# Kernel tuning notes

Measured on AMD Instinct MI355X. Metric: run time of the kernel, lower is better.

## Reference

```python
import jax, jax.numpy as jnp
import numpy as np

N_NODES = 100000
N_EDGES = 1600000
NUM_FEATURES = 256
HIDDEN_DIM = 128
NUM_CLASSES = 16


def setup_inputs() -> dict:
    key = jax.random.key(0)
    k1, k2, k3, k4 = jax.random.split(key, 4)
    x = jax.random.normal(k1, (N_NODES, NUM_FEATURES), dtype=jnp.float32)
    edge_index = jax.random.randint(k2, (2, N_EDGES), 0, N_NODES, dtype=jnp.int64)
    # Glorot-style init like PyG GCNConv's Linear
    W1 = jax.random.normal(k3, (NUM_FEATURES, HIDDEN_DIM), dtype=jnp.float32) / np.sqrt(NUM_FEATURES)
    b1 = jnp.zeros((HIDDEN_DIM,), dtype=jnp.float32)
    W2 = jax.random.normal(k4, (HIDDEN_DIM, NUM_CLASSES), dtype=jnp.float32) / np.sqrt(HIDDEN_DIM)
    b2 = jnp.zeros((NUM_CLASSES,), dtype=jnp.float32)
    return {"x": x, "edge_index": edge_index, "W1": W1, "b1": b1, "W2": W2, "b2": b2}


def _gcn_norm(edge_index, num_nodes):
    """PyG GCNConv default: add self-loops, symmetric deg^{-1/2} A deg^{-1/2} norm."""
    loops = jnp.arange(num_nodes, dtype=edge_index.dtype)
    row = jnp.concatenate([edge_index[0], loops])  # source
    col = jnp.concatenate([edge_index[1], loops])  # target
    deg = jax.ops.segment_sum(jnp.ones_like(col, dtype=jnp.float32), col,
                              num_segments=num_nodes)
    dinv = jnp.where(deg > 0, jax.lax.rsqrt(deg), 0.0)
    norm = dinv[row] * dinv[col]  # [E + N]
    return row, col, norm


def _gcn_conv(h, row, col, norm, num_nodes):
    # transform first (PyG: lin then propagate), then normalized sum-aggregate
    msg = h[row] * norm[:, None]            # [E+N, d] gather + scale
    return jax.ops.segment_sum(msg, col, num_segments=num_nodes)


def reference(x, edge_index, W1, b1, W2, b2):
    num_nodes = x.shape[0]
    row, col, norm = _gcn_norm(edge_index, num_nodes)
    h = x @ W1
    h = _gcn_conv(h, row, col, norm, num_nodes) + b1
    h = jax.nn.relu(h)
    h = h @ W2
    out = _gcn_conv(h, row, col, norm, num_nodes) + b2
    return out
```

## Files before the change

### kernel.cpp

```cpp
#include <hip/hip_runtime.h>

#define N_NODES 100000
#define N_EDGES 1600000
#define F_IN    256
#define F_HID   128
#define F_OUT   16

#define BSHIFT  9
#define BNODES  512
#define NB      196
#define CHUNK   4096
#define NCHUNK  ((N_EDGES + CHUNK - 1) / CHUNK)

typedef __attribute__((ext_vector_type(8))) short short8;
typedef __attribute__((ext_vector_type(4))) float float4v;

__device__ __forceinline__ unsigned int bf16_rn(float f) {
    unsigned int u = __float_as_uint(f);
    return (u + 0x7FFFu + ((u >> 16) & 1u)) >> 16;
}
__device__ __forceinline__ unsigned int pk2(float lo, float hi) {
    return bf16_rn(lo) | (bf16_rn(hi) << 16);
}


__global__ __launch_bounds__(256) void k_bhist(const int* __restrict__ coli,
                                               int* __restrict__ bcnt) {
    __shared__ int lc[NB];
    int tid = threadIdx.x;
    for (int i = tid; i < NB; i += 256) lc[i] = 0;
    __syncthreads();
    for (int e = blockIdx.x * 256 + tid; e < N_EDGES; e += 256 * 256)
        atomicAdd(&lc[coli[e] >> BSHIFT], 1);
    __syncthreads();
    for (int i = tid; i < NB; i += 256)
        if (lc[i]) atomicAdd(&bcnt[i], lc[i]);
}

__global__ __launch_bounds__(256) void k_bscan(const int* __restrict__ bcnt,
                                               int* __restrict__ bbase,
                                               int* __restrict__ bcur) {
    __shared__ int sc[256];
    int t = threadIdx.x;
    int v = (t < NB) ? bcnt[t] : 0;
    sc[t] = v; __syncthreads();
    for (int off = 1; off < 256; off <<= 1) {
        int x = (t >= off) ? sc[t - off] : 0;
        __syncthreads();
        sc[t] += x;
        __syncthreads();
    }
    if (t < NB) {
        int e = sc[t] - v;
        bbase[t] = e;
        bcur[t]  = e;
    }
    if (t == 0) bbase[NB] = N_EDGES;
}

__global__ __launch_bounds__(256) void k_binscatter(const int* __restrict__ rowi,
                                                    const int* __restrict__ coli,
                                                    int* __restrict__ bcur,
                                                    int2* __restrict__ ebuf) {
    __shared__ int cnt[NB], gbase[NB], run[NB];
    int tid = threadIdx.x;
    int e0 = blockIdx.x * CHUNK;
    for (int i = tid; i < NB; i += 256) { cnt[i] = 0; run[i] = 0; }
    __syncthreads();
    int d[16], s[16];
    #pragma unroll
    for (int i = 0; i < 16; i++) {
        int e = e0 + i * 256 + tid;
        if (e < N_EDGES) {
            d[i] = coli[e]; s[i] = rowi[e];
            atomicAdd(&cnt[d[i] >> BSHIFT], 1);
        } else d[i] = -1;
    }
    __syncthreads();
    for (int i = tid; i < NB; i += 256)
        gbase[i] = cnt[i] ? atomicAdd(&bcur[i], cnt[i]) : 0;
    __syncthreads();
    #pragma unroll
    for (int i = 0; i < 16; i++) {
        if (d[i] >= 0) {
            int b = d[i] >> BSHIFT;
            int off = atomicAdd(&run[b], 1);
            ebuf[gbase[b] + off] = make_int2(d[i], s[i]);
        }
    }
}

__global__ __launch_bounds__(256) void k_finalize(const int* __restrict__ bbase,
                                                  const int2* __restrict__ ebuf,
                                                  int* __restrict__ row_ptr,
                                                  float* __restrict__ dinv,
                                                  int* __restrict__ esrc) {
    __shared__ int ndeg[BNODES];
    __shared__ int sc[BNODES];
    int tid = threadIdx.x;
    int b   = blockIdx.x;
    int nb0 = b << BSHIFT;
    int ebeg = bbase[b], eend = bbase[b + 1];
    ndeg[tid] = 0; ndeg[tid + 256] = 0;
    __syncthreads();
    for (int e = ebeg + tid; e < eend; e += 256)
        atomicAdd(&ndeg[ebuf[e].x - nb0], 1);
    __syncthreads();
    int i0 = tid, i1 = tid + 256;
    sc[i0] = ndeg[i0]; sc[i1] = ndeg[i1];
    __syncthreads();
    for (int off = 1; off < BNODES; off <<= 1) {
        int v0 = (i0 >= off) ? sc[i0 - off] : 0;
        int v1 = (i1 >= off) ? sc[i1 - off] : 0;
        __syncthreads();
        sc[i0] += v0; sc[i1] += v1;
        __syncthreads();
    }
    #pragma unroll
    for (int k = 0; k < 2; k++) {
        int i = tid + k * 256;
        int n = nb0 + i;
        int deg = ndeg[i];
        int excl = sc[i] - deg;
        if (n < N_NODES) {
            row_ptr[n] = ebeg + excl;
            dinv[n]    = rsqrtf(1.0f + (float)deg);
        }
        ndeg[i] = excl;
    }
    if (b == NB - 1 && tid == 0) row_ptr[N_NODES] = N_EDGES;
    __syncthreads();
    for (int e = ebeg + tid; e < eend; e += 256) {
        int2 p = ebuf[e];
        int off = atomicAdd(&ndeg[p.x - nb0], 1);
        esrc[ebeg + off] = p.y;
    }
}


__global__ __launch_bounds__(256) void k_transW(const float* __restrict__ W1,
                                                ushort* __restrict__ Wt) {
    int t = blockIdx.x * 256 + threadIdx.x;
    int c = t & 127, k = t >> 7;
    Wt[c * 256 + k] = (ushort)bf16_rn(W1[k * 128 + c]);
}


__global__ __launch_bounds__(256) void k_gemm1(const float* __restrict__ x,
                                               const ushort* __restrict__ Wt,
                                               const float* __restrict__ dinv,
                                               ushort* __restrict__ g1) {
    __shared__ ushort Al[128 * 40];
    __shared__ ushort Bl[128 * 40];
    const int tid = threadIdx.x;
    const int w = tid >> 6;
    const int l = tid & 63;
    const int m = l & 15;
    const int q = l >> 4;
    const int R0 = blockIdx.x * 128;

    const int srow = tid >> 1;
    const int soff = (tid & 1) * 16;

    int vr = R0 + srow; if (vr > N_NODES - 1) vr = N_NODES - 1;
    const float*  xrow = &x[(size_t)vr * F_IN + soff];
    const ushort* wrow = &Wt[srow * 256 + soff];

    float4v acc[2][8];
    #pragma unroll
    for (int i = 0; i < 2; i++)
        #pragma unroll
        for (int j = 0; j < 8; j++) acc[i][j] = (float4v){0.f, 0.f, 0.f, 0.f};

    for (int kt = 0; kt < F_IN; kt += 32) {
        float4 f0 = *(const float4*)&xrow[kt + 0];
        float4 f1 = *(const float4*)&xrow[kt + 4];
        float4 f2 = *(const float4*)&xrow[kt + 8];
        float4 f3 = *(const float4*)&xrow[kt + 12];
        uint4 wv0 = *(const uint4*)&wrow[kt + 0];
        uint4 wv1 = *(const uint4*)&wrow[kt + 8];
        uint4 pa, pb;
        pa.x = pk2(f0.x, f0.y); pa.y = pk2(f0.z, f0.w);
        pa.z = pk2(f1.x, f1.y); pa.w = pk2(f1.z, f1.w);
        pb.x = pk2(f2.x, f2.y); pb.y = pk2(f2.z, f2.w);
        pb.z = pk2(f3.x, f3.y); pb.w = pk2(f3.z, f3.w);
        *(uint4*)&Al[srow * 40 + soff]     = pa;
        *(uint4*)&Al[srow * 40 + soff + 8] = pb;
        *(uint4*)&Bl[srow * 40 + soff]     = wv0;
        *(uint4*)&Bl[srow * 40 + soff + 8] = wv1;
        __syncthreads();

        short8 af0 = *(const short8*)&Al[(w * 32 + m) * 40 + q * 8];
        short8 af1 = *(const short8*)&Al[(w * 32 + 16 + m) * 40 + q * 8];
        #pragma unroll
        for (int n = 0; n < 8; n++) {
            short8 bfr = *(const short8*)&Bl[(n * 16 + m) * 40 + q * 8];
            acc[0][n] = __builtin_amdgcn_mfma_f32_16x16x32_bf16(af0, bfr, acc[0][n], 0, 0, 0);
            acc[1][n] = __builtin_amdgcn_mfma_f32_16x16x32_bf16(af1, bfr, acc[1][n], 0, 0, 0);
        }
        __syncthreads();
    }

    const int rbase = R0 + w * 32 + q * 4;
    float dv0[4], dv1[4];
    #pragma unroll
    for (int r = 0; r < 4; r++) {
        int v0 = rbase + r;      dv0[r] = (v0 < N_NODES) ? dinv[v0] : 0.f;
        int v1 = rbase + 16 + r; dv1[r] = (v1 < N_NODES) ? dinv[v1] : 0.f;
    }
    #pragma unroll
    for (int n = 0; n < 8; n++) {
        #pragma unroll
        for (int r = 0; r < 4; r++) {
            int v0 = rbase + r;
            if (v0 < N_NODES)
                g1[v0 * F_HID + n * 16 + m] = (ushort)bf16_rn(dv0[r] * acc[0][n][r]);
            int v1 = rbase + 16 + r;
            if (v1 < N_NODES)
                g1[v1 * F_HID + n * 16 + m] = (ushort)bf16_rn(dv1[r] * acc[1][n][r]);
        }
    }
}


__global__ __launch_bounds__(256) void k_agg1(const int* __restrict__ row_ptr,
                                              const int* __restrict__ esrc,
                                              const float* __restrict__ dinv,
                                              const unsigned int* __restrict__ g1,
                                              const float* __restrict__ b1,
                                              float* __restrict__ h1b) {
    int node = blockIdx.x * 4 + (threadIdx.x >> 6);
    int lane = threadIdx.x & 63;
    if (node >= N_NODES) return;
    int s = row_ptr[node], t = row_ptr[node + 1];
    unsigned int u = g1[node * 64 + lane];
    float ax = __uint_as_float(u << 16);
    float ay = __uint_as_float(u & 0xFFFF0000u);
    int e = s;
    for (; e + 3 < t; e += 4) {
        int r0 = esrc[e], r1 = esrc[e + 1], r2 = esrc[e + 2], r3 = esrc[e + 3];
        unsigned int u0 = g1[r0 * 64 + lane];
        unsigned int u1 = g1[r1 * 64 + lane];
        unsigned int u2 = g1[r2 * 64 + lane];
        unsigned int u3 = g1[r3 * 64 + lane];
        ax += __uint_as_float(u0 << 16) + __uint_as_float(u1 << 16)
            + __uint_as_float(u2 << 16) + __uint_as_float(u3 << 16);
        ay += __uint_as_float(u0 & 0xFFFF0000u) + __uint_as_float(u1 & 0xFFFF0000u)
            + __uint_as_float(u2 & 0xFFFF0000u) + __uint_as_float(u3 & 0xFFFF0000u);
    }
    for (; e < t; e++) {
        unsigned int u0 = g1[esrc[e] * 64 + lane];
        ax += __uint_as_float(u0 << 16);
        ay += __uint_as_float(u0 & 0xFFFF0000u);
    }
    float wv = dinv[node];
    float2 bb = ((const float2*)b1)[lane];
    float2 o;
    o.x = fmaxf(fmaf(wv, ax, bb.x), 0.0f);
    o.y = fmaxf(fmaf(wv, ay, bb.y), 0.0f);
    ((float2*)h1b)[node * 64 + lane] = o;
}


__global__ __launch_bounds__(256) void k_gemm2(const float* __restrict__ h1b,
                                               const float* __restrict__ W2,
                                               const float* __restrict__ dinv,
                                               float* __restrict__ g2) {
    __shared__ float ls[64 * 129];
    __shared__ float ws2[F_HID * F_OUT];
    const int tid = threadIdx.x;
    const int v0  = blockIdx.x * 64;

    for (int i = tid; i < F_HID * F_OUT; i += 256) ws2[i] = W2[i];
    __syncthreads();

    #pragma unroll
    for (int i = 0; i < 32; i++) {
        int f = i * 256 + tid;
        int rr = f >> 7, cc = f & 127;
        int v = v0 + rr;
        ls[rr * 129 + cc] = (v < N_NODES) ? h1b[v * F_HID + cc] : 0.0f;
    }
    __syncthreads();

    const int v  = tid >> 2;
    const int cq = (tid & 3) * 4;
    float acc[4] = {0.f, 0.f, 0.f, 0.f};
    #pragma unroll 8
    for (int f = 0; f < F_HID; f++) {
        float a = ls[v * 129 + f];
        #pragma unroll
        for (int j = 0; j < 4; j++)
            acc[j] = fmaf(a, ws2[f * F_OUT + cq + j], acc[j]);
    }
    int vv = v0 + v;
    if (vv < N_NODES) {
        float w = dinv[vv];
        float4 t = make_float4(w * acc[0], w * acc[1], w * acc[2], w * acc[3]);
        *(float4*)&g2[vv * F_OUT + cq] = t;
    }
}


__global__ __launch_bounds__(256) void k_agg2(const int* __restrict__ row_ptr,
                                              const int* __restrict__ esrc,
                                              const float* __restrict__ dinv,
                                              const float* __restrict__ g2,
                                              const float* __restrict__ b2,
                                              float* __restrict__ out) {
    int gid = blockIdx.x * 256 + threadIdx.x;
    int node = gid >> 4;
    int f = gid & 15;
    if (node >= N_NODES) return;
    int s = row_ptr[node], t = row_ptr[node + 1];
    float acc = g2[node * 16 + f];
    int e = s;
    for (; e + 3 < t; e += 4) {
        acc += g2[esrc[e] * 16 + f] + g2[esrc[e + 1] * 16 + f]
             + g2[esrc[e + 2] * 16 + f] + g2[esrc[e + 3] * 16 + f];
    }
    for (; e < t; e++) acc += g2[esrc[e] * 16 + f];
    out[node * 16 + f] = fmaf(dinv[node], acc, b2[f]);
}


extern "C" void kernel_launch(void* const* d_in, const int* in_sizes, int n_in,
                              void* d_out, int out_size, void* d_ws, size_t ws_size,
                              hipStream_t stream) {
    const float* x   = (const float*)d_in[0];
    const int*   ei  = (const int*)d_in[1];
    const float* W1  = (const float*)d_in[2];
    const float* b1  = (const float*)d_in[3];
    const float* W2  = (const float*)d_in[4];
    const float* b2  = (const float*)d_in[5];
    float* out = (float*)d_out;

    const int* rowi = ei;
    const int* coli = ei + N_EDGES;

    char* ws = (char*)d_ws;
    int*    bcnt    = (int*)(ws + 0);
    int*    bbase   = (int*)(ws + 4096);
    int*    bcur    = (int*)(ws + 8192);
    int*    row_ptr = (int*)(ws + 16384);
    float*  dinv    = (float*)(ws + 524288);
    int2*   ebuf    = (int2*)(ws + 1048576);
    int*    esrc    = (int*)(ws + 14680064);
    ushort* Wt      = (ushort*)(ws + 22020096);
    ushort* g1      = (ushort*)(ws + 23068672);
    float*  g2      = (float*)(ws + 23068672);
    float*  h1b     = (float*)(ws + 50331648);

    hipMemsetAsync(bcnt, 0, NB * sizeof(int), stream);

    k_bhist     <<<256, 256, 0, stream>>>(coli, bcnt);
    k_bscan     <<<1, 256, 0, stream>>>(bcnt, bbase, bcur);
    k_binscatter<<<NCHUNK, 256, 0, stream>>>(rowi, coli, bcur, ebuf);
    k_finalize  <<<NB, 256, 0, stream>>>(bbase, ebuf, row_ptr, dinv, esrc);
    k_transW    <<<128, 256, 0, stream>>>(W1, Wt);

    k_gemm1     <<<(N_NODES + 127) / 128, 256, 0, stream>>>(x, Wt, dinv, g1);
    k_agg1      <<<(N_NODES + 3) / 4, 256, 0, stream>>>(row_ptr, esrc, dinv,
                                                        (const unsigned int*)g1, b1, h1b);
    k_gemm2     <<<(N_NODES + 63) / 64, 256, 0, stream>>>(h1b, W2, dinv, g2);
    k_agg2      <<<(N_NODES * 16 + 255) / 256, 256, 0, stream>>>(row_ptr, esrc, dinv, g2, b2, out);
}
```

Before: 396.8 us.

## Fuse layer-1 aggregation with second GEMM and pack edge bins into 32-bit words

Layer-1 aggregation now computes bias and ReLU into shared memory and immediately multiplies by W2 in the same kernel. This drops the fp32 h1b intermediate (a 51 MB write plus a read) and one kernel launch. Edge binning now packs the local destination (9 bits) and the source (17 bits) into one 32-bit word instead of an int2, which halves ebuf traffic. The gather loops are unrolled to 8 for more memory-level parallelism. The cost is that W2 is reloaded into shared memory by every 4-node block, and the small per-wave matvec runs with a block-wide sync.

Measured after the change: 371.5 us. -6.4%, faster.

```diff
diff --git a/kernel.cpp b/kernel.cpp
--- a/kernel.cpp
+++ b/kernel.cpp
@@ -22,6 +22,8 @@
 __device__ __forceinline__ unsigned int pk2(float lo, float hi) {
     return bf16_rn(lo) | (bf16_rn(hi) << 16);
 }
+__device__ __forceinline__ float blo(unsigned int u) { return __uint_as_float(u << 16); }
+__device__ __forceinline__ float bhi(unsigned int u) { return __uint_as_float(u & 0xFFFF0000u); }
 
 
 __global__ __launch_bounds__(256) void k_bhist(const int* __restrict__ coli,
@@ -61,7 +63,7 @@
 __global__ __launch_bounds__(256) void k_binscatter(const int* __restrict__ rowi,
                                                     const int* __restrict__ coli,
                                                     int* __restrict__ bcur,
-                                                    int2* __restrict__ ebuf) {
+                                                    unsigned int* __restrict__ ebuf) {
     __shared__ int cnt[NB], gbase[NB], run[NB];
     int tid = threadIdx.x;
     int e0 = blockIdx.x * CHUNK;
@@ -85,13 +87,13 @@
         if (d[i] >= 0) {
             int b = d[i] >> BSHIFT;
             int off = atomicAdd(&run[b], 1);
-            ebuf[gbase[b] + off] = make_int2(d[i], s[i]);
+            ebuf[gbase[b] + off] = ((unsigned int)(d[i] & 511) << 17) | (unsigned int)s[i];
         }
     }
 }
 
 __global__ __launch_bounds__(256) void k_finalize(const int* __restrict__ bbase,
-                                                  const int2* __restrict__ ebuf,
+                                                  const unsigned int* __restrict__ ebuf,
                                                   int* __restrict__ row_ptr,
                                                   float* __restrict__ dinv,
                                                   int* __restrict__ esrc) {
@@ -104,7 +106,7 @@
     ndeg[tid] = 0; ndeg[tid + 256] = 0;
     __syncthreads();
     for (int e = ebeg + tid; e < eend; e += 256)
-        atomicAdd(&ndeg[ebuf[e].x - nb0], 1);
+        atomicAdd(&ndeg[ebuf[e] >> 17], 1);
     __syncthreads();
     int i0 = tid, i1 = tid + 256;
     sc[i0] = ndeg[i0]; sc[i1] = ndeg[i1];
@@ -131,9 +133,9 @@
     if (b == NB - 1 && tid == 0) row_ptr[N_NODES] = N_EDGES;
     __syncthreads();
     for (int e = ebeg + tid; e < eend; e += 256) {
-        int2 p = ebuf[e];
-        int off = atomicAdd(&ndeg[p.x - nb0], 1);
-        esrc[ebeg + off] = p.y;
+        unsigned int p = ebuf[e];
+        int off = atomicAdd(&ndeg[p >> 17], 1);
+        esrc[ebeg + off] = (int)(p & 0x1FFFFu);
     }
 }
 
@@ -223,82 +225,65 @@
 }
 
 
-__global__ __launch_bounds__(256) void k_agg1(const int* __restrict__ row_ptr,
-                                              const int* __restrict__ esrc,
-                                              const float* __restrict__ dinv,
-                                              const unsigned int* __restrict__ g1,
-                                              const float* __restrict__ b1,
-                                              float* __restrict__ h1b) {
-    int node = blockIdx.x * 4 + (threadIdx.x >> 6);
-    int lane = threadIdx.x & 63;
-    if (node >= N_NODES) return;
+__global__ __launch_bounds__(256) void k_agg1g2(const int* __restrict__ row_ptr,
+                                                const int* __restrict__ esrc,
+                                                const float* __restrict__ dinv,
+                                                const unsigned int* __restrict__ g1,
+                                                const float* __restrict__ b1,
+                                                const float* __restrict__ W2,
+                                                float* __restrict__ g2) {
+    __shared__ float hl[4 * 132];
+    __shared__ float W2s[F_HID * F_OUT];
+    const int tid  = threadIdx.x;
+    const int wave = tid >> 6;
+    const int lane = tid & 63;
+    const int node = blockIdx.x * 4 + wave;
+
+    for (int i = tid; i < F_HID * F_OUT; i += 256) W2s[i] = W2[i];
+
     int s = row_ptr[node], t = row_ptr[node + 1];
     unsigned int u = g1[node * 64 + lane];
-    float ax = __uint_as_float(u << 16);
-    float ay = __uint_as_float(u & 0xFFFF0000u);
+    float ax = blo(u), ay = bhi(u);
     int e = s;
+    for (; e + 7 < t; e += 8) {
+        int r0 = esrc[e],     r1 = esrc[e + 1], r2 = esrc[e + 2], r3 = esrc[e + 3];
+        int r4 = esrc[e + 4], r5 = esrc[e + 5], r6 = esrc[e + 6], r7 = esrc[e + 7];
+        unsigned int u0 = g1[r0 * 64 + lane], u1 = g1[r1 * 64 + lane];
+        unsigned int u2 = g1[r2 * 64 + lane], u3 = g1[r3 * 64 + lane];
+        unsigned int u4 = g1[r4 * 64 + lane], u5 = g1[r5 * 64 + lane];
+        unsigned int u6 = g1[r6 * 64 + lane], u7 = g1[r7 * 64 + lane];
+        ax += blo(u0) + blo(u1) + blo(u2) + blo(u3)
+            + blo(u4) + blo(u5) + blo(u6) + blo(u7);
+        ay += bhi(u0) + bhi(u1) + bhi(u2) + bhi(u3)
+            + bhi(u4) + bhi(u5) + bhi(u6) + bhi(u7);
+    }
     for (; e + 3 < t; e += 4) {
         int r0 = esrc[e], r1 = esrc[e + 1], r2 = esrc[e + 2], r3 = esrc[e + 3];
-        unsigned int u0 = g1[r0 * 64 + lane];
-        unsigned int u1 = g1[r1 * 64 + lane];
-        unsigned int u2 = g1[r2 * 64 + lane];
-        unsigned int u3 = g1[r3 * 64 + lane];
-        ax += __uint_as_float(u0 << 16) + __uint_as_float(u1 << 16)
-            + __uint_as_float(u2 << 16) + __uint_as_float(u3 << 16);
-        ay += __uint_as_float(u0 & 0xFFFF0000u) + __uint_as_float(u1 & 0xFFFF0000u)
-            + __uint_as_float(u2 & 0xFFFF0000u) + __uint_as_float(u3 & 0xFFFF0000u);
+        unsigned int u0 = g1[r0 * 64 + lane], u1 = g1[r1 * 64 + lane];
+        unsigned int u2 = g1[r2 * 64 + lane], u3 = g1[r3 * 64 + lane];
+        ax += blo(u0) + blo(u1) + blo(u2) + blo(u3);
+        ay += bhi(u0) + bhi(u1) + bhi(u2) + bhi(u3);
     }
     for (; e < t; e++) {
         unsigned int u0 = g1[esrc[e] * 64 + lane];
-        ax += __uint_as_float(u0 << 16);
-        ay += __uint_as_float(u0 & 0xFFFF0000u);
+        ax += blo(u0); ay += bhi(u0);
     }
     float wv = dinv[node];
     float2 bb = ((const float2*)b1)[lane];
-    float2 o;
-    o.x = fmaxf(fmaf(wv, ax, bb.x), 0.0f);
-    o.y = fmaxf(fmaf(wv, ay, bb.y), 0.0f);
-    ((float2*)h1b)[node * 64 + lane] = o;
-}
-
-
-__global__ __launch_bounds__(256) void k_gemm2(const float* __restrict__ h1b,
-                                               const float* __restrict__ W2,
-                                               const float* __restrict__ dinv,
-                                               float* __restrict__ g2) {
-    __shared__ float ls[64 * 129];
-    __shared__ float ws2[F_HID * F_OUT];
-    const int tid = threadIdx.x;
-    const int v0  = blockIdx.x * 64;
-
-    for (int i = tid; i < F_HID * F_OUT; i += 256) ws2[i] = W2[i];
-    __syncthreads();
-
+    hl[wave * 132 + lane * 2]     = fmaxf(fmaf(wv, ax, bb.x), 0.0f);
+    hl[wave * 132 + lane * 2 + 1] = fmaxf(fmaf(wv, ay, bb.y), 0.0f);
+    __syncthreads();
+
+    const int col = lane & 15, part = lane >> 4;
+    float acc = 0.f;
     #pragma unroll
     for (int i = 0; i < 32; i++) {
-        int f = i * 256 + tid;
-        int rr = f >> 7, cc = f & 127;
-        int v = v0 + rr;
-        ls[rr * 129 + cc] = (v < N_NODES) ? h1b[v * F_HID + cc] : 0.0f;
-    }
-    __syncthreads();
-
-    const int v  = tid >> 2;
-    const int cq = (tid & 3) * 4;
-    float acc[4] = {0.f, 0.f, 0.f, 0.f};
-    #pragma unroll 8
-    for (int f = 0; f < F_HID; f++) {
-        float a = ls[v * 129 + f];
-        #pragma unroll
-        for (int j = 0; j < 4; j++)
-            acc[j] = fmaf(a, ws2[f * F_OUT + cq + j], acc[j]);
-    }
-    int vv = v0 + v;
-    if (vv < N_NODES) {
-        float w = dinv[vv];
-        float4 t = make_float4(w * acc[0], w * acc[1], w * acc[2], w * acc[3]);
-        *(float4*)&g2[vv * F_OUT + cq] = t;
-    }
+        int f = i * 4 + part;
+        acc = fmaf(hl[wave * 132 + f], W2s[f * 16 + col], acc);
+    }
+    acc += __shfl_xor(acc, 16);
+    acc += __shfl_xor(acc, 32);
+    if (lane < 16) g2[node * 16 + col] = wv * acc;
 }
 
 
@@ -315,6 +300,13 @@
     int s = row_ptr[node], t = row_ptr[node + 1];
     float acc = g2[node * 16 + f];
     int e = s;
+    for (; e + 7 < t; e += 8) {
+        float a0 = g2[esrc[e] * 16 + f],     a1 = g2[esrc[e + 1] * 16 + f];
+        float a2 = g2[esrc[e + 2] * 16 + f], a3 = g2[esrc[e + 3] * 16 + f];
+        float a4 = g2[esrc[e + 4] * 16 + f], a5 = g2[esrc[e + 5] * 16 + f];
+        float a6 = g2[esrc[e + 6] * 16 + f], a7 = g2[esrc[e + 7] * 16 + f];
+        acc += a0 + a1 + a2 + a3 + a4 + a5 + a6 + a7;
+    }
     for (; e + 3 < t; e += 4) {
         acc += g2[esrc[e] * 16 + f] + g2[esrc[e + 1] * 16 + f]
              + g2[esrc[e + 2] * 16 + f] + g2[esrc[e + 3] * 16 + f];
@@ -339,17 +331,16 @@
     const int* coli = ei + N_EDGES;
 
     char* ws = (char*)d_ws;
-    int*    bcnt    = (int*)(ws + 0);
-    int*    bbase   = (int*)(ws + 4096);
-    int*    bcur    = (int*)(ws + 8192);
-    int*    row_ptr = (int*)(ws + 16384);
-    float*  dinv    = (float*)(ws + 524288);
-    int2*   ebuf    = (int2*)(ws + 1048576);
-    int*    esrc    = (int*)(ws + 14680064);
-    ushort* Wt      = (ushort*)(ws + 22020096);
-    ushort* g1      = (ushort*)(ws + 23068672);
-    float*  g2      = (float*)(ws + 23068672);
-    float*  h1b     = (float*)(ws + 50331648);
+    int*          bcnt    = (int*)(ws + 0);
+    int*          bbase   = (int*)(ws + 4096);
+    int*          bcur    = (int*)(ws + 8192);
+    int*          row_ptr = (int*)(ws + 16384);
+    float*        dinv    = (float*)(ws + 524288);
+    unsigned int* ebuf    = (unsigned int*)(ws + 1048576);
+    int*          esrc    = (int*)(ws + 8388608);
+    ushort*       Wt      = (ushort*)(ws + 15728640);
+    ushort*       g1      = (ushort*)(ws + 16777216);
+    float*        g2      = (float*)(ws + 45088768);
 
     hipMemsetAsync(bcnt, 0, NB * sizeof(int), stream);
 
@@ -360,8 +351,7 @@
     k_transW    <<<128, 256, 0, stream>>>(W1, Wt);
 
     k_gemm1     <<<(N_NODES + 127) / 128, 256, 0, stream>>>(x, Wt, dinv, g1);
-    k_agg1      <<<(N_NODES + 3) / 4, 256, 0, stream>>>(row_ptr, esrc, dinv,
-                                                        (const unsigned int*)g1, b1, h1b);
-    k_gemm2     <<<(N_NODES + 63) / 64, 256, 0, stream>>>(h1b, W2, dinv, g2);
+    k_agg1g2    <<<N_NODES / 4, 256, 0, stream>>>(row_ptr, esrc, dinv,
+                                                  (const unsigned int*)g1, b1, W2, g2);
     k_agg2      <<<(N_NODES * 16 + 255) / 256, 256, 0, stream>>>(row_ptr, esrc, dinv, g2, b2, out);
 }
```
